# Performance work log

Hardware: AMD Instinct MI355X
Metric: run time of the kernel (lower is better)

Reference implementation:

```python
import jax, jax.numpy as jnp
import numpy as np

N = 50000      # num nodes
DIN = 256
DOUT = 256
E = 400000     # edges per sign
NEG_SLOPE = 0.2  # LeakyReLU(0.2)


def setup_inputs() -> dict:
    key = jax.random.key(0)
    ks = jax.random.split(key, 12)
    p = lambda k, shp: jax.random.normal(k, shp, jnp.float32) * 0.05
    return {
        "node_reps": jax.random.normal(ks[0], (N, DIN), jnp.float32),
        "adj_pos": jax.random.randint(ks[1], (2, E), 0, N, dtype=jnp.int32),
        "adj_neg": jax.random.randint(ks[2], (2, E), 0, N, dtype=jnp.int32),
        "basis": p(ks[3], (2, DIN, DOUT)),        # num_bases=num_relations=2
        "att": p(ks[4], (2, 2)),
        "mapping_func": p(ks[5], (1, 2 * DOUT)),
        "bias": p(ks[6], (1, DOUT)),
        "theta1": p(ks[7], (DOUT, DOUT)),          # HGNN_conv 1 linear weight
        "b1": jnp.zeros((DOUT,), jnp.float32),
        "theta2": p(ks[8], (DOUT, DOUT)),          # HGNN_conv 2 linear weight
        "b2": jnp.zeros((DOUT,), jnp.float32),
    }


def reference(node_reps, adj_pos, adj_neg, basis, att, mapping_func, bias,
              theta1, b1, theta2, b2):
    # basis-decomposed relation weights: Wr[r] = sum_b att[r,b] * basis[b]
    Wr = (att @ basis.reshape(2, -1)).reshape(2, DIN, DOUT)
    h_pos = node_reps @ Wr[0]
    h_neg = node_reps @ Wr[1]
    # HGNN_conv feature transforms (linear + bias)
    h_pos = h_pos @ theta1 + b1
    h_neg = h_neg @ theta2 + b2

    # edge attention score: mapping_func . concat(h[src], h[dst])
    w_src = mapping_func[0, :DOUT]
    w_dst = mapping_func[0, DOUT:]
    e_pos = h_pos[adj_pos[0]] @ w_src + h_pos[adj_pos[1]] @ w_dst  # [E]
    e_neg = h_neg[adj_neg[0]] @ w_src + h_neg[adj_neg[1]] @ w_dst  # [E]
    e_all = jnp.concatenate([e_pos, e_neg])                         # [2E]
    coeff = jax.nn.sigmoid(jnp.where(e_all > 0, e_all, NEG_SLOPE * e_all))

    # symmetric degree normalization over the union graph
    rows_all = jnp.concatenate([adj_pos[0], adj_neg[0]])
    cols_all = jnp.concatenate([adj_pos[1], adj_neg[1]])
    deg = jnp.sqrt(jax.ops.segment_sum(
        jnp.ones_like(coeff), rows_all, num_segments=N))            # [N]
    coeff = coeff / (deg[rows_all] * deg[cols_all])

    # sparse aggregation (SpecialSpmm): out[r] += coeff_e * h[c]
    h_agg_pos = jax.ops.segment_sum(
        coeff[:E, None] * h_pos[adj_pos[1]], adj_pos[0], num_segments=N)
    h_agg_neg = jax.ops.segment_sum(
        coeff[E:, None] * h_neg[adj_neg[1]], adj_neg[0], num_segments=N)

    output = h_agg_pos - h_agg_neg + bias
    return (output, h_agg_pos, h_agg_neg)
```

## Files before the change

kernel.cpp:

```cpp
#include <hip/hip_runtime.h>

#define N_NODES 50000
#define NEDGE   400000
#define SB      512
#define NSB     ((N_NODES + SB - 1) / SB)
#define H8SCALE 128.0f

typedef __bf16 bf16x8 __attribute__((ext_vector_type(8)));
typedef float  f32x4  __attribute__((ext_vector_type(4)));
typedef float  f32x2  __attribute__((ext_vector_type(2)));
typedef unsigned short u16x8 __attribute__((ext_vector_type(8)));
typedef int    i32x2  __attribute__((ext_vector_type(2)));

#define GLDS16(gp, lp) \
  __builtin_amdgcn_global_load_lds((const __attribute__((address_space(1))) void*)(gp), \
                                   (__attribute__((address_space(3))) void*)(lp), 16, 0, 0)

static __device__ __forceinline__ unsigned short f2bf(float f) {
  unsigned u = __float_as_uint(f);
  unsigned r = (u + 0x7fffu + ((u >> 16) & 1u)) >> 16;
  return (unsigned short)r;
}
static __device__ __forceinline__ float bf2f(unsigned short v) {
  return __uint_as_float((unsigned)v << 16);
}

__global__ __launch_bounds__(256) void fused0_kernel(
    const float* __restrict__ basis, const float* __restrict__ att,
    const float* __restrict__ theta1, const float* __restrict__ theta2,
    const float* __restrict__ bias1, const float* __restrict__ bias2,
    unsigned short* __restrict__ Wt, float* __restrict__ biasvec,
    const float* __restrict__ node, unsigned short* __restrict__ A16,
    const int* __restrict__ adjp, const int* __restrict__ adjn,
    int* __restrict__ cntp, int* __restrict__ cntn) {
  const int b = blockIdx.x;
  if (b < 512) {
    const int r = b >> 8, k = b & 255;
    const int n = threadIdx.x;
    const float a0 = att[r * 2 + 0], a1 = att[r * 2 + 1];
    const float* th = (r == 0) ? theta1 : theta2;
    const float* b0 = basis + k * 256;
    const float* b1p = basis + 65536 + k * 256;
    float ac0 = 0.f, ac1 = 0.f, ac2 = 0.f, ac3 = 0.f;
    for (int j = 0; j < 256; j += 4) {
      const float w0 = a0 * b0[j + 0] + a1 * b1p[j + 0];
      const float w1 = a0 * b0[j + 1] + a1 * b1p[j + 1];
      const float w2 = a0 * b0[j + 2] + a1 * b1p[j + 2];
      const float w3 = a0 * b0[j + 3] + a1 * b1p[j + 3];
      ac0 += w0 * th[(j + 0) * 256 + n];
      ac1 += w1 * th[(j + 1) * 256 + n];
      ac2 += w2 * th[(j + 2) * 256 + n];
      ac3 += w3 * th[(j + 3) * 256 + n];
    }
    Wt[(size_t)(r * 256 + n) * 256 + k] = f2bf((ac0 + ac1) + (ac2 + ac3));
    if (k == 0) biasvec[r * 256 + n] = (r == 0) ? bias1[n] : bias2[n];
  } else if (b < 2560) {
    const long total = (long)N_NODES * 256 / 4;
    long idx = (long)(b - 512) * 256 + threadIdx.x;
    const long stride = 2048L * 256;
    for (; idx < total; idx += stride) {
      const f32x4 v = __builtin_nontemporal_load(&((const f32x4*)node)[idx]);
      ushort4 o;
      o.x = f2bf(v.x); o.y = f2bf(v.y); o.z = f2bf(v.z); o.w = f2bf(v.w);
      ((ushort4*)A16)[idx] = o;
    }
  } else {
    const int g = (b - 2560) * 256 + threadIdx.x;
    if (g < NEDGE) atomicAdd(&cntp[adjp[g]], 1);
    else if (g < 2 * NEDGE) atomicAdd(&cntn[adjn[g - NEDGE]], 1);
  }
}

__global__ __launch_bounds__(256) void gemm_kernel(
    const unsigned short* __restrict__ A,
    const unsigned short* __restrict__ Wt,
    const float* __restrict__ biasvec,
    const float* __restrict__ mapping,
    unsigned char* __restrict__ H8,
    float* __restrict__ sdbuf) {
  __shared__ unsigned short smem[128 * 136];
  unsigned short* sA = smem;
  unsigned short* sB = smem + 8192;
  const int tid = threadIdx.x;
  const int wave = tid >> 6, lane = tid & 63;
  const int wm = wave >> 1, wn = wave & 1;
  const int bid = blockIdx.y * 4 + blockIdx.x;
  const int xcd = bid & 7, loc = bid >> 3;
  const int nq = 1564 >> 3, nr = 1564 & 7;
  const int swz = (xcd < nr ? xcd * (nq + 1) : nr * (nq + 1) + (xcd - nr) * nq) + loc;
  const int m0 = (swz >> 2) * 128;
  const int n0 = (swz & 3) * 128;

  f32x4 acc[4][4];
#pragma unroll
  for (int a = 0; a < 4; ++a)
#pragma unroll
    for (int b = 0; b < 4; ++b) acc[a][b] = (f32x4){0.f, 0.f, 0.f, 0.f};

  const int srow = lane >> 3;
  const int skel = ((lane & 7) ^ srow) << 3;

  for (int ks = 0; ks < 4; ++ks) {
    const int kg = ks * 64 + skel;
#pragma unroll
    for (int c = 0; c < 4; ++c) {
      const int chunk = wave * 4 + c;
      const int row = chunk * 8 + srow;
      int rowg = m0 + row;
      rowg = rowg < N_NODES ? rowg : N_NODES - 1;
      GLDS16(A + (size_t)rowg * 256 + kg, sA + chunk * 512);
      GLDS16(Wt + (size_t)(n0 + row) * 256 + kg, sB + chunk * 512);
    }
    __syncthreads();
#pragma unroll
    for (int kk = 0; kk < 2; ++kk) {
      const int kb = (kk * 32 + ((lane >> 4) << 3)) << 1;
      bf16x8 af[4], bfr[4];
#pragma unroll
      for (int m16 = 0; m16 < 4; ++m16) {
        const int row = wm * 64 + m16 * 16 + (lane & 15);
        af[m16] = *(const bf16x8*)((const char*)sA + row * 128 + (kb ^ ((row & 7) << 4)));
      }
#pragma unroll
      for (int n16 = 0; n16 < 4; ++n16) {
        const int col = wn * 64 + n16 * 16 + (lane & 15);
        bfr[n16] = *(const bf16x8*)((const char*)sB + col * 128 + (kb ^ ((col & 7) << 4)));
      }
#pragma unroll
      for (int m16 = 0; m16 < 4; ++m16)
#pragma unroll
        for (int n16 = 0; n16 < 4; ++n16)
          acc[m16][n16] = __builtin_amdgcn_mfma_f32_16x16x32_bf16(af[m16], bfr[n16], acc[m16][n16], 0, 0, 0);
    }
    __syncthreads();
  }

  const bool sgn = (n0 >= 256);
  const int nb = (sgn ? (n0 - 256) : n0) >> 7;
  const int slice = nb * 2 + wn;
  float* __restrict__ sS = sdbuf + ((size_t)((sgn ? 2 : 0) + 0) * 4 + slice) * N_NODES;
  float* __restrict__ sD = sdbuf + ((size_t)((sgn ? 2 : 0) + 1) * 4 + slice) * N_NODES;
  float bv[4], wsv[4], wdv[4];
#pragma unroll
  for (int n16 = 0; n16 < 4; ++n16) {
    const int colg = n0 + wn * 64 + n16 * 16 + (lane & 15);
    bv[n16] = biasvec[colg];
    const int cm = colg & 255;
    wsv[n16] = mapping[cm];
    wdv[n16] = mapping[256 + cm];
  }
#pragma unroll
  for (int m16 = 0; m16 < 4; ++m16) {
    const int rowb = wm * 64 + m16 * 16 + ((lane >> 4) << 2);
#pragma unroll
    for (int j = 0; j < 4; ++j) {
      const int rowl = rowb + j;
      float vs = 0.f, vd = 0.f;
#pragma unroll
      for (int n16 = 0; n16 < 4; ++n16) {
        const float v = acc[m16][n16][j] + bv[n16];
        const int coll = wn * 64 + n16 * 16 + (lane & 15);
        smem[rowl * 136 + coll] = f2bf(v);
        vs += v * wsv[n16];
        vd += v * wdv[n16];
      }
#pragma unroll
      for (int off = 1; off < 16; off <<= 1) { vs += __shfl_xor(vs, off); vd += __shfl_xor(vd, off); }
      const int rowg = m0 + rowl;
      if ((lane & 15) == 0 && rowg < N_NODES) { sS[rowg] = vs; sD[rowg] = vd; }
    }
  }
  __syncthreads();
#pragma unroll
  for (int it = 0; it < 8; ++it) {
    const int row = it * 16 + (tid >> 4);
    const int c8 = (tid & 15) * 8;
    const int rowg = m0 + row;
    if (rowg < N_NODES) {
      const u16x8 v = *(const u16x8*)(smem + row * 136 + c8);
      float f[8];
#pragma unroll
      for (int q = 0; q < 8; ++q) f[q] = bf2f((unsigned short)v[q]) * H8SCALE;
      int w0 = __builtin_amdgcn_cvt_pk_fp8_f32(f[0], f[1], 0, false);
      w0     = __builtin_amdgcn_cvt_pk_fp8_f32(f[2], f[3], w0, true);
      int w1 = __builtin_amdgcn_cvt_pk_fp8_f32(f[4], f[5], 0, false);
      w1     = __builtin_amdgcn_cvt_pk_fp8_f32(f[6], f[7], w1, true);
      i32x2 o; o.x = w0; o.y = w1;
      *(i32x2*)(&H8[(size_t)rowg * 512 + n0 + c8]) = o;
    }
  }
}

__global__ __launch_bounds__(SB) void scan1_kernel(const int* __restrict__ cntp,
                                                   const int* __restrict__ cntn,
                                                   int* __restrict__ bsp, int* __restrict__ bsn) {
  __shared__ int lp[SB / 64], ln[SB / 64];
  const int i = blockIdx.x * SB + threadIdx.x;
  int vp = (i < N_NODES) ? cntp[i] : 0;
  int vn = (i < N_NODES) ? cntn[i] : 0;
#pragma unroll
  for (int off = 1; off < 64; off <<= 1) { vp += __shfl_xor(vp, off); vn += __shfl_xor(vn, off); }
  const int wave = threadIdx.x >> 6, lane = threadIdx.x & 63;
  if (lane == 0) { lp[wave] = vp; ln[wave] = vn; }
  __syncthreads();
  if (threadIdx.x == 0) {
    int ap = 0, an = 0;
#pragma unroll
    for (int w = 0; w < SB / 64; ++w) { ap += lp[w]; an += ln[w]; }
    bsp[blockIdx.x] = ap; bsn[blockIdx.x] = an;
  }
}

__global__ __launch_bounds__(SB) void scan3_kernel(const int* __restrict__ cntp,
                                                   const int* __restrict__ cntn,
                                                   const int* __restrict__ bsp,
                                                   const int* __restrict__ bsn,
                                                   const float* __restrict__ sdbuf,
                                                   int* __restrict__ rsp, int* __restrict__ rsn,
                                                   int* __restrict__ curp, int* __restrict__ curn,
                                                   f32x4* __restrict__ nip, f32x4* __restrict__ nin) {
  __shared__ int sp_[SB], sn_[SB];
  __shared__ int pbs[128], nbs[128];
  const int t = threadIdx.x;
  if (t < 128) {
    pbs[t] = (t < NSB) ? bsp[t] : 0;
    nbs[t] = (t < NSB) ? bsn[t] : 0;
  }
  __syncthreads();
  for (int off = 1; off < 128; off <<= 1) {
    const int ap = (t >= off && t < 128) ? pbs[t - off] : 0;
    const int an = (t >= off && t < 128) ? nbs[t - off] : 0;
    __syncthreads();
    if (t < 128) { pbs[t] += ap; nbs[t] += an; }
    __syncthreads();
  }
  const int basep = (blockIdx.x == 0) ? 0 : pbs[blockIdx.x - 1];
  const int basen = (blockIdx.x == 0) ? 0 : nbs[blockIdx.x - 1];
  if (blockIdx.x == 0 && t == 0) { rsp[N_NODES] = pbs[127]; rsn[N_NODES] = nbs[127]; }

  const int i = blockIdx.x * SB + t;
  const int cp = (i < N_NODES) ? cntp[i] : 0;
  const int cn = (i < N_NODES) ? cntn[i] : 0;
  sp_[t] = cp; sn_[t] = cn;
  __syncthreads();
  for (int off = 1; off < SB; off <<= 1) {
    const int ap = (t >= off) ? sp_[t - off] : 0;
    const int an = (t >= off) ? sn_[t - off] : 0;
    __syncthreads();
    sp_[t] += ap; sn_[t] += an;
    __syncthreads();
  }
  if (i < N_NODES) {
    const int rp = basep + sp_[t] - cp;
    const int rn = basen + sn_[t] - cn;
    rsp[i] = rp; curp[i] = rp;
    rsn[i] = rn; curn[i] = rn;
    const float rdeg = 1.f / sqrtf((float)(cp + cn));
    float sp4 = 0.f, dp4 = 0.f, sn4 = 0.f, dn4 = 0.f;
#pragma unroll
    for (int sl = 0; sl < 4; ++sl) {
      sp4 += sdbuf[(size_t)(0 * 4 + sl) * N_NODES + i];
      dp4 += sdbuf[(size_t)(1 * 4 + sl) * N_NODES + i];
      sn4 += sdbuf[(size_t)(2 * 4 + sl) * N_NODES + i];
      dn4 += sdbuf[(size_t)(3 * 4 + sl) * N_NODES + i];
    }
    nip[i] = (f32x4){sp4, dp4, rdeg, 0.f};
    nin[i] = (f32x4){sn4, dn4, rdeg, 0.f};
  }
}

__global__ void scatter_kernel(const int* __restrict__ adjp, const int* __restrict__ adjn,
                               int* __restrict__ curp, int* __restrict__ curn,
                               int* __restrict__ colp, int* __restrict__ coln) {
  const int g = blockIdx.x * blockDim.x + threadIdx.x;
  if (g >= 2 * NEDGE) return;
  if (g < NEDGE) {
    const int src = adjp[g];
    colp[atomicAdd(&curp[src], 1)] = adjp[NEDGE + g];
  } else {
    const int e2 = g - NEDGE;
    const int src = adjn[e2];
    coln[atomicAdd(&curn[src], 1)] = adjn[NEDGE + e2];
  }
}

__global__ __launch_bounds__(256) void agg_kernel(
    const unsigned char* __restrict__ H8,
    const int* __restrict__ rsp, const int* __restrict__ colp,
    const int* __restrict__ rsn, const int* __restrict__ coln,
    const f32x4* __restrict__ nip, const f32x4* __restrict__ nin,
    const float* __restrict__ bias, float* __restrict__ out) {
  __shared__ f32x4 sneg[2][64];
  const int wave = threadIdx.x >> 6, lane = threadIdx.x & 63;
  const int r = wave >> 1;
  const int sign = wave & 1;
  const int i = blockIdx.x * 2 + r;
  const int* __restrict__ rs  = sign ? rsn : rsp;
  const int* __restrict__ col = sign ? coln : colp;
  const f32x4* __restrict__ ni = sign ? nin : nip;
  const unsigned char* __restrict__ Hb = H8 + sign * 256 + (size_t)lane * 4;
  const f32x4 me = ni[i];
  const float srow = me.x;
  const float rdrow = me.z * (1.0f / H8SCALE);
  const int beg = rs[i], end = rs[i + 1];
  f32x4 a0 = {0,0,0,0}, a1 = {0,0,0,0}, a2 = {0,0,0,0}, a3 = {0,0,0,0};
  for (int chunk = beg; chunk < end; chunk += 64) {
    const int m = (end - chunk < 64) ? end - chunk : 64;
    int cv = 0;
    float fv = 0.f;
    if (lane < m) {
      cv = __builtin_nontemporal_load(&col[chunk + lane]);
      const f32x4 nb = ni[cv];
      const float e = srow + nb.y;
      const float l = e > 0.f ? e : 0.2f * e;
      fv = (1.f / (1.f + expf(-l))) * rdrow * nb.z;
    }
    int k = 0;
    for (; k + 4 <= m; k += 4) {
      const int   c0 = __shfl(cv, k),     c1 = __shfl(cv, k + 1);
      const int   c2 = __shfl(cv, k + 2), c3 = __shfl(cv, k + 3);
      const float f0 = __shfl(fv, k),     f1 = __shfl(fv, k + 1);
      const float f2 = __shfl(fv, k + 2), f3 = __shfl(fv, k + 3);
      const unsigned w0 = *(const unsigned*)(Hb + (size_t)c0 * 512);
      const unsigned w1 = *(const unsigned*)(Hb + (size_t)c1 * 512);
      const unsigned w2 = *(const unsigned*)(Hb + (size_t)c2 * 512);
      const unsigned w3 = *(const unsigned*)(Hb + (size_t)c3 * 512);
      const f32x2 l0 = __builtin_amdgcn_cvt_pk_f32_fp8(w0, false), h0 = __builtin_amdgcn_cvt_pk_f32_fp8(w0, true);
      const f32x2 l1 = __builtin_amdgcn_cvt_pk_f32_fp8(w1, false), h1 = __builtin_amdgcn_cvt_pk_f32_fp8(w1, true);
      const f32x2 l2 = __builtin_amdgcn_cvt_pk_f32_fp8(w2, false), h2 = __builtin_amdgcn_cvt_pk_f32_fp8(w2, true);
      const f32x2 l3 = __builtin_amdgcn_cvt_pk_f32_fp8(w3, false), h3 = __builtin_amdgcn_cvt_pk_f32_fp8(w3, true);
      a0.x += f0 * l0.x; a0.y += f0 * l0.y; a0.z += f0 * h0.x; a0.w += f0 * h0.y;
      a1.x += f1 * l1.x; a1.y += f1 * l1.y; a1.z += f1 * h1.x; a1.w += f1 * h1.y;
      a2.x += f2 * l2.x; a2.y += f2 * l2.y; a2.z += f2 * h2.x; a2.w += f2 * h2.y;
      a3.x += f3 * l3.x; a3.y += f3 * l3.y; a3.z += f3 * h3.x; a3.w += f3 * h3.y;
    }
    for (; k < m; ++k) {
      const int   c0 = __shfl(cv, k);
      const float f0 = __shfl(fv, k);
      const unsigned w0 = *(const unsigned*)(Hb + (size_t)c0 * 512);
      const f32x2 l0 = __builtin_amdgcn_cvt_pk_f32_fp8(w0, false), h0 = __builtin_amdgcn_cvt_pk_f32_fp8(w0, true);
      a0.x += f0 * l0.x; a0.y += f0 * l0.y; a0.z += f0 * h0.x; a0.w += f0 * h0.y;
    }
  }
  f32x4 a = (a0 + a1) + (a2 + a3);
  if (sign) sneg[r][lane] = a;
  __syncthreads();
  if (sign) {
    __builtin_nontemporal_store(a, ((f32x4*)(out + (size_t)2 * N_NODES * 256)) + (size_t)i * 64 + lane);
  } else {
    const f32x4 an = sneg[r][lane];
    const f32x4 bv = ((const f32x4*)bias)[lane];
    const f32x4 o = a - an + bv;
    __builtin_nontemporal_store(o, ((f32x4*)out) + (size_t)i * 64 + lane);
    __builtin_nontemporal_store(a, ((f32x4*)(out + (size_t)N_NODES * 256)) + (size_t)i * 64 + lane);
  }
}

extern "C" void kernel_launch(void* const* d_in, const int* in_sizes, int n_in,
                              void* d_out, int out_size, void* d_ws, size_t ws_size,
                              hipStream_t stream) {
  const float* node    = (const float*)d_in[0];
  const int*   adjp    = (const int*)d_in[1];
  const int*   adjn    = (const int*)d_in[2];
  const float* basis   = (const float*)d_in[3];
  const float* att     = (const float*)d_in[4];
  const float* mapping = (const float*)d_in[5];
  const float* bias    = (const float*)d_in[6];
  const float* theta1  = (const float*)d_in[7];
  const float* b1      = (const float*)d_in[8];
  const float* theta2  = (const float*)d_in[9];
  const float* b2      = (const float*)d_in[10];
  float* out = (float*)d_out;

  size_t off = 0;
  char* wsb = (char*)d_ws;
  auto alloc = [&](size_t bytes) -> char* {
    char* p = wsb + off;
    off = (off + bytes + 255) & ~(size_t)255;
    return p;
  };
  unsigned short* A16 = (unsigned short*)alloc((size_t)N_NODES * 256 * 2);
  unsigned char*  H8  = (unsigned char*)alloc((size_t)N_NODES * 512);
  unsigned short* Wt  = (unsigned short*)alloc(512 * 256 * 2);
  float* biasvec = (float*)alloc(512 * 4);
  float* sdbuf = (float*)alloc((size_t)16 * N_NODES * 4);
  f32x4* nip = (f32x4*)alloc((size_t)N_NODES * 16);
  f32x4* nin = (f32x4*)alloc((size_t)N_NODES * 16);
  int* cnt2 = (int*)alloc((size_t)2 * N_NODES * 4);
  int* cntp = cnt2, *cntn = cnt2 + N_NODES;
  int* cur2 = (int*)alloc((size_t)2 * N_NODES * 4);
  int* curp = cur2, *curn = cur2 + N_NODES;
  int* rsp = (int*)alloc((N_NODES + 1) * 4);
  int* rsn = (int*)alloc((N_NODES + 1) * 4);
  int* bsp = (int*)alloc(NSB * 4);
  int* bsn = (int*)alloc(NSB * 4);
  int* colp = (int*)alloc((size_t)NEDGE * 4);
  int* coln = (int*)alloc((size_t)NEDGE * 4);

  (void)hipMemsetAsync(cnt2, 0, (size_t)2 * N_NODES * 4, stream);

  fused0_kernel<<<512 + 2048 + (2 * NEDGE) / 256, 256, 0, stream>>>(
      basis, att, theta1, theta2, b1, b2, Wt, biasvec, node, A16, adjp, adjn, cntp, cntn);
  gemm_kernel<<<dim3(4, 391), 256, 0, stream>>>(A16, Wt, biasvec, mapping, H8, sdbuf);
  scan1_kernel<<<NSB, SB, 0, stream>>>(cntp, cntn, bsp, bsn);
  scan3_kernel<<<NSB, SB, 0, stream>>>(cntp, cntn, bsp, bsn, sdbuf, rsp, rsn, curp, curn, nip, nin);
  scatter_kernel<<<(2 * NEDGE) / 256, 256, 0, stream>>>(adjp, adjn, curp, curn, colp, coln);
  agg_kernel<<<N_NODES / 2, 256, 0, stream>>>(H8, rsp, colp, rsn, coln, nip, nin, bias, out);
}
```

Measured before the change: 213.3 us.

## Fuse CSR scan and edge scatter into one cooperative kernel with grid syncs

Merges the two scan kernels and the edge-scatter kernel into a single cooperative launch of NSB (98) blocks, using grid.sync() between phases in place of kernel boundaries. This removes two launches and their inter-kernel gaps. In exchange, the scatter phase now runs with only 98 blocks striding over 800K edges instead of a wide grid, and grid-wide syncs have their own cost.

After: 252.7 us. +18.5%, slower.

```diff
diff --git a/kernel.cpp b/kernel.cpp
--- a/kernel.cpp
+++ b/kernel.cpp
@@ -1,4 +1,7 @@
 #include <hip/hip_runtime.h>
+#include <hip/hip_cooperative_groups.h>
+
+namespace cg = cooperative_groups;
 
 #define N_NODES 50000
 #define NEDGE   400000
@@ -191,37 +194,38 @@
   }
 }
 
-__global__ __launch_bounds__(SB) void scan1_kernel(const int* __restrict__ cntp,
-                                                   const int* __restrict__ cntn,
-                                                   int* __restrict__ bsp, int* __restrict__ bsn) {
-  __shared__ int lp[SB / 64], ln[SB / 64];
-  const int i = blockIdx.x * SB + threadIdx.x;
-  int vp = (i < N_NODES) ? cntp[i] : 0;
-  int vn = (i < N_NODES) ? cntn[i] : 0;
-#pragma unroll
-  for (int off = 1; off < 64; off <<= 1) { vp += __shfl_xor(vp, off); vn += __shfl_xor(vn, off); }
-  const int wave = threadIdx.x >> 6, lane = threadIdx.x & 63;
-  if (lane == 0) { lp[wave] = vp; ln[wave] = vn; }
-  __syncthreads();
-  if (threadIdx.x == 0) {
-    int ap = 0, an = 0;
-#pragma unroll
-    for (int w = 0; w < SB / 64; ++w) { ap += lp[w]; an += ln[w]; }
-    bsp[blockIdx.x] = ap; bsn[blockIdx.x] = an;
-  }
-}
-
-__global__ __launch_bounds__(SB) void scan3_kernel(const int* __restrict__ cntp,
-                                                   const int* __restrict__ cntn,
-                                                   const int* __restrict__ bsp,
-                                                   const int* __restrict__ bsn,
-                                                   const float* __restrict__ sdbuf,
-                                                   int* __restrict__ rsp, int* __restrict__ rsn,
-                                                   int* __restrict__ curp, int* __restrict__ curn,
-                                                   f32x4* __restrict__ nip, f32x4* __restrict__ nin) {
+__global__ __launch_bounds__(SB) void csr_kernel(
+    const int* __restrict__ cntp, const int* __restrict__ cntn,
+    int* __restrict__ bsp, int* __restrict__ bsn,
+    const float* __restrict__ sdbuf,
+    int* __restrict__ rsp, int* __restrict__ rsn,
+    int* __restrict__ curp, int* __restrict__ curn,
+    f32x4* __restrict__ nip, f32x4* __restrict__ nin,
+    const int* __restrict__ adjp, const int* __restrict__ adjn,
+    int* __restrict__ colp, int* __restrict__ coln) {
+  cg::grid_group grid = cg::this_grid();
   __shared__ int sp_[SB], sn_[SB];
   __shared__ int pbs[128], nbs[128];
   const int t = threadIdx.x;
+  const int i = blockIdx.x * SB + t;
+
+  {
+    int vp = (i < N_NODES) ? cntp[i] : 0;
+    int vn = (i < N_NODES) ? cntn[i] : 0;
+#pragma unroll
+    for (int off = 1; off < 64; off <<= 1) { vp += __shfl_xor(vp, off); vn += __shfl_xor(vn, off); }
+    const int wv = t >> 6, lane = t & 63;
+    if (lane == 0) { sp_[wv] = vp; sn_[wv] = vn; }
+    __syncthreads();
+    if (t == 0) {
+      int ap = 0, an = 0;
+#pragma unroll
+      for (int w = 0; w < SB / 64; ++w) { ap += sp_[w]; an += sn_[w]; }
+      bsp[blockIdx.x] = ap; bsn[blockIdx.x] = an;
+    }
+  }
+  grid.sync();
+
   if (t < 128) {
     pbs[t] = (t < NSB) ? bsp[t] : 0;
     nbs[t] = (t < NSB) ? bsn[t] : 0;
@@ -238,7 +242,6 @@
   const int basen = (blockIdx.x == 0) ? 0 : nbs[blockIdx.x - 1];
   if (blockIdx.x == 0 && t == 0) { rsp[N_NODES] = pbs[127]; rsn[N_NODES] = nbs[127]; }
 
-  const int i = blockIdx.x * SB + t;
   const int cp = (i < N_NODES) ? cntp[i] : 0;
   const int cn = (i < N_NODES) ? cntn[i] : 0;
   sp_[t] = cp; sn_[t] = cn;
@@ -267,20 +270,18 @@
     nip[i] = (f32x4){sp4, dp4, rdeg, 0.f};
     nin[i] = (f32x4){sn4, dn4, rdeg, 0.f};
   }
-}
-
-__global__ void scatter_kernel(const int* __restrict__ adjp, const int* __restrict__ adjn,
-                               int* __restrict__ curp, int* __restrict__ curn,
-                               int* __restrict__ colp, int* __restrict__ coln) {
-  const int g = blockIdx.x * blockDim.x + threadIdx.x;
-  if (g >= 2 * NEDGE) return;
-  if (g < NEDGE) {
-    const int src = adjp[g];
-    colp[atomicAdd(&curp[src], 1)] = adjp[NEDGE + g];
-  } else {
-    const int e2 = g - NEDGE;
-    const int src = adjn[e2];
-    coln[atomicAdd(&curn[src], 1)] = adjn[NEDGE + e2];
+  grid.sync();
+
+  const int stride = gridDim.x * SB;
+  for (int g = blockIdx.x * SB + t; g < 2 * NEDGE; g += stride) {
+    if (g < NEDGE) {
+      const int src = adjp[g];
+      colp[atomicAdd(&curp[src], 1)] = adjp[NEDGE + g];
+    } else {
+      const int e2 = g - NEDGE;
+      const int src = adjn[e2];
+      coln[atomicAdd(&curn[src], 1)] = adjn[NEDGE + e2];
+    }
   }
 }
 
@@ -402,8 +403,12 @@
   fused0_kernel<<<512 + 2048 + (2 * NEDGE) / 256, 256, 0, stream>>>(
       basis, att, theta1, theta2, b1, b2, Wt, biasvec, node, A16, adjp, adjn, cntp, cntn);
   gemm_kernel<<<dim3(4, 391), 256, 0, stream>>>(A16, Wt, biasvec, mapping, H8, sdbuf);
-  scan1_kernel<<<NSB, SB, 0, stream>>>(cntp, cntn, bsp, bsn);
-  scan3_kernel<<<NSB, SB, 0, stream>>>(cntp, cntn, bsp, bsn, sdbuf, rsp, rsn, curp, curn, nip, nin);
-  scatter_kernel<<<(2 * NEDGE) / 256, 256, 0, stream>>>(adjp, adjn, curp, curn, colp, coln);
+  {
+    void* cargs[] = {(void*)&cntp, (void*)&cntn, (void*)&bsp, (void*)&bsn, (void*)&sdbuf,
+                     (void*)&rsp, (void*)&rsn, (void*)&curp, (void*)&curn,
+                     (void*)&nip, (void*)&nin, (void*)&adjp, (void*)&adjn,
+                     (void*)&colp, (void*)&coln};
+    (void)hipLaunchCooperativeKernel((void*)csr_kernel, dim3(NSB), dim3(SB), cargs, 0, stream);
+  }
   agg_kernel<<<N_NODES / 2, 256, 0, stream>>>(H8, rsp, colp, rsn, coln, nip, nin, bias, out);
 }
```
